# Kernel optimization log

Measured on AMD Instinct MI355X. Metric: run time of the kernel, lower is better.

The kernel has to match this reference:

```python
import jax, jax.numpy as jnp
import numpy as np


def setup_inputs() -> dict:
    key = jax.random.key(0)
    k1, k2, k3 = jax.random.split(key, 3)
    B, C_in, H, W = 32, 128, 56, 56
    C_out, ksz = 256, 3
    x = jax.random.normal(k1, (B, C_in, H, W), dtype=jnp.float32)
    weight = jax.random.normal(k2, (C_out, C_in, ksz, ksz), dtype=jnp.float32) * 0.05
    bias = jax.random.normal(k3, (C_out,), dtype=jnp.float32)
    return {"x": x, "weight": weight, "bias": bias}


PADDING = 1
GROUPS = 1


def reference(x, weight, bias):
    # Same math as the manual pad+unfold+einsum: a standard stride-1 grouped
    # conv2d with symmetric zero padding. Expressed as implicit-GEMM conv.
    out = jax.lax.conv_general_dilated(
        x, weight,
        window_strides=(1, 1),
        padding=[(PADDING, PADDING), (PADDING, PADDING)],
        dimension_numbers=("NCHW", "OIHW", "NCHW"),
        feature_group_count=GROUPS,
    )
    out = out + bias[None, :, None, None]
    return out
```

## Files before the change

kernel.cpp:

```cpp
#include <hip/hip_runtime.h>
#include <stdint.h>

#define BATCH 32
#define CIN   128
#define HH    56
#define WW    56
#define COUT  256
#define HP    58
#define WP    58

typedef __attribute__((ext_vector_type(8))) short short8;
typedef __attribute__((ext_vector_type(4))) float floatx4;

#define GLOAD_LDS16(gptr, lptr)                                          \
  __builtin_amdgcn_global_load_lds(                                      \
      (const __attribute__((address_space(1))) void*)(gptr),             \
      (__attribute__((address_space(3))) void*)(lptr), 16, 0, 0)

__device__ __forceinline__ unsigned short f32_to_bf16(float f) {
  unsigned int u = __float_as_uint(f);
  u = u + 0x7fffu + ((u >> 16) & 1u);
  return (unsigned short)(u >> 16);
}
__device__ __forceinline__ unsigned int pack2(float a, float b) {
  return (unsigned int)f32_to_bf16(a) | ((unsigned int)f32_to_bf16(b) << 16);
}


__global__ void pad_transpose_kernel(const float* __restrict__ x,
                                     unsigned short* __restrict__ xpt) {
  const int blk = blockIdx.x;
  const int b = blk / HP;
  const int i = blk - b * HP;
  const int t = threadIdx.x;
  unsigned short* dst = xpt + (size_t)blk * (WP * CIN);

  if (i == 0 || i == HP - 1) {
    const uint4 z = {0, 0, 0, 0};
    for (int idx = t; idx < 928; idx += 256)
      *(uint4*)(dst + (size_t)idx * 8) = z;
    return;
  }

  __shared__ float tile[CIN * 59];
  tile[(t >> 1) * 59 + (t & 1) * 57] = 0.0f;
  {
    const int ci = t >> 1;
    const int seg = t & 1;
    const float* row =
        x + (((size_t)b * CIN + ci) * HH + (i - 1)) * WW + seg * 28;
    float* trow = tile + ci * 59 + 1 + seg * 28;
#pragma unroll
    for (int q = 0; q < 7; ++q) {
      const float4 v = *(const float4*)(row + q * 4);
      trow[q * 4 + 0] = v.x;
      trow[q * 4 + 1] = v.y;
      trow[q * 4 + 2] = v.z;
      trow[q * 4 + 3] = v.w;
    }
  }
  __syncthreads();
  for (int idx = t; idx < 928; idx += 256) {
    const int j = idx >> 4;
    const int ci0 = (idx & 15) * 8;
    uint4 pk;
    pk.x = pack2(tile[(ci0 + 0) * 59 + j], tile[(ci0 + 1) * 59 + j]);
    pk.y = pack2(tile[(ci0 + 2) * 59 + j], tile[(ci0 + 3) * 59 + j]);
    pk.z = pack2(tile[(ci0 + 4) * 59 + j], tile[(ci0 + 5) * 59 + j]);
    pk.w = pack2(tile[(ci0 + 6) * 59 + j], tile[(ci0 + 7) * 59 + j]);
    *(uint4*)(dst + (size_t)idx * 8) = pk;
  }
}

__global__ void weight_transpose_kernel(const float* __restrict__ wsrc,
                                        unsigned short* __restrict__ wt) {
  const int o8 = blockIdx.x * 256 + threadIdx.x;
  const int r = o8 >> 12;
  const int rem = o8 & 4095;
  const int co = rem >> 4;
  const int ci0 = (rem & 15) * 8;
  const float* s = wsrc + ((size_t)co * CIN + ci0) * 9 + r;
  uint4 pk;
  pk.x = pack2(s[0 * 9], s[1 * 9]);
  pk.y = pack2(s[2 * 9], s[3 * 9]);
  pk.z = pack2(s[4 * 9], s[5 * 9]);
  pk.w = pack2(s[6 * 9], s[7 * 9]);
  *(uint4*)(wt + (size_t)o8 * 8) = pk;
}

__global__ __launch_bounds__(256, 2) void conv_gemm_kernel(
    const unsigned short* __restrict__ xpt,
    const unsigned short* __restrict__ wt,
    const float* __restrict__ bias,
    float* __restrict__ out) {
  __shared__ __align__(16) uint32_t smem[16384];
  short* const S = (short*)smem;
  float* const ep = (float*)smem;

  const int g = blockIdx.x;
  const int xcd = g & 7;
  const int jj = g >> 3;
  const int nt = jj & 1;
  const int mt = (jj >> 1) * 8 + xcd;
  const int b = mt / 28;
  const int h0 = (mt - b * 28) * 2;
  const int co0 = nt * 128;

  const int t = threadIdx.x;
  const int lane = t & 63;
  const int wv = t >> 6;
  const int mw = wv & 1;
  const int nw = wv >> 1;
  const int laneM = lane & 15;
  const int laneKg = lane >> 4;
  const int sw = (laneM & 3) ^ ((laneM >> 2) & 3);
  const int xk = (laneKg ^ sw) * 8;
  const int rowreg = laneKg * 4;

  const unsigned short* ag[2];
  const unsigned short* bg[2];
#pragma unroll
  for (int c = 0; c < 2; ++c) {
    const int u = c * 256 + t;
    const int mm = u >> 2;
    const int smm = (mm & 3) ^ ((mm >> 2) & 3);
    const int j8 = (((u & 3) ^ smm) * 8);
    const int hp0 = h0 + (mm >> 6);
    const int wc0 = mm & 63;
    ag[c] = xpt + ((size_t)((b * HP + hp0) * WP + wc0)) * CIN + j8;
    bg[c] = wt + (size_t)(co0 + mm) * CIN + j8;
  }
  const int dA = wv * 512;

  floatx4 acc[4][4] = {};

  auto stageK = [&](int kk) {
    const int r = kk >> 2;
    const int dh = (r * 11) >> 5;
    const int dw = r - dh * 3;
    const int aoff = (dh * WP + dw) * CIN + (kk & 3) * 32;
    const int boff = r * (COUT * CIN) + (kk & 3) * 32;
    short* const base = S + (kk & 3) * 8192;
    GLOAD_LDS16(ag[0] + aoff, base + dA);
    GLOAD_LDS16(ag[1] + aoff, base + 2048 + dA);
    GLOAD_LDS16(bg[0] + boff, base + 4096 + dA);
    GLOAD_LDS16(bg[1] + boff, base + 4096 + 2048 + dA);
  };

  stageK(0);
  stageK(1);
  asm volatile("s_waitcnt vmcnt(4)" ::: "memory");
  __builtin_amdgcn_s_barrier();
  __builtin_amdgcn_sched_barrier(0);

  for (int kk = 0; kk < 36; ++kk) {
    const short* Ab = S + (kk & 3) * 8192;
    const short* Bb = Ab + 4096;
    short8 af[4], bfr[4];
#pragma unroll
    for (int mi = 0; mi < 4; ++mi)
      af[mi] = *(const short8*)&Ab[(mw * 64 + mi * 16 + laneM) * 32 + xk];
#pragma unroll
    for (int ni = 0; ni < 4; ++ni)
      bfr[ni] = *(const short8*)&Bb[(nw * 64 + ni * 16 + laneM) * 32 + xk];
    if (kk < 34) stageK(kk + 2);
    __builtin_amdgcn_s_setprio(1);
#pragma unroll
    for (int mi = 0; mi < 4; ++mi)
#pragma unroll
      for (int ni = 0; ni < 4; ++ni)
        acc[mi][ni] = __builtin_amdgcn_mfma_f32_16x16x32_bf16(
            af[mi], bfr[ni], acc[mi][ni], 0, 0, 0);
    __builtin_amdgcn_s_setprio(0);
    if (kk < 34)
      asm volatile("s_waitcnt vmcnt(4)" ::: "memory");
    else
      asm volatile("s_waitcnt vmcnt(0)" ::: "memory");
    __builtin_amdgcn_s_barrier();
    __builtin_amdgcn_sched_barrier(0);
  }

  for (int ni = 0; ni < 4; ++ni) {
    __syncthreads();
#pragma unroll
    for (int mi = 0; mi < 4; ++mi)
      *(float4*)&ep[(nw * 16 + laneM) * 132 + mw * 64 + mi * 16 + rowreg] =
          *(float4*)&acc[mi][ni];
    __syncthreads();
#pragma unroll
    for (int rr = 0; rr < 16; ++rr) {
      const int rowid = wv * 16 + rr;
      const int cg = rowid >> 1;
      const int hh = rowid & 1;
      const int co = co0 + (cg >> 4) * 64 + ni * 16 + (cg & 15);
      const float bv = bias[co];
      if (lane < WW) {
        out[(((size_t)b * COUT + co) * HH + h0 + hh) * WW + lane] =
            ep[cg * 132 + hh * 64 + lane] + bv;
      }
    }
  }
}

__global__ void naive_conv_kernel(const float* __restrict__ x,
                                  const float* __restrict__ wgt,
                                  const float* __restrict__ bias,
                                  float* __restrict__ out, long n) {
  long idx = (long)blockIdx.x * 256 + threadIdx.x;
  if (idx >= n) return;
  int w = (int)(idx % WW);
  long q = idx / WW;
  int h = (int)(q % HH);
  q /= HH;
  int co = (int)(q % COUT);
  int b = (int)(q / COUT);
  float s = bias[co];
  for (int ci = 0; ci < CIN; ++ci) {
    const float* xp = x + (((size_t)b * CIN + ci) * HH) * WW;
    const float* wp = wgt + ((size_t)co * CIN + ci) * 9;
    for (int dh = 0; dh < 3; ++dh) {
      int hh = h + dh - 1;
      if (hh < 0 || hh >= HH) continue;
      for (int dw = 0; dw < 3; ++dw) {
        int ww2 = w + dw - 1;
        if (ww2 < 0 || ww2 >= WW) continue;
        s += xp[hh * WW + ww2] * wp[dh * 3 + dw];
      }
    }
  }
  out[idx] = s;
}

extern "C" void kernel_launch(void* const* d_in, const int* in_sizes, int n_in,
                              void* d_out, int out_size, void* d_ws,
                              size_t ws_size, hipStream_t stream) {
  const float* x = (const float*)d_in[0];
  const float* wgt = (const float*)d_in[1];
  const float* bias = (const float*)d_in[2];
  float* out = (float*)d_out;

  const size_t XPT = (size_t)BATCH * HP * WP * CIN;
  const size_t SLACK = 1024;
  const size_t WT = (size_t)9 * COUT * CIN;
  const size_t need = (XPT + SLACK + WT) * sizeof(unsigned short);

  if (ws_size >= need) {
    unsigned short* xpt = (unsigned short*)d_ws;
    unsigned short* wtp = xpt + XPT + SLACK;
    hipLaunchKernelGGL(pad_transpose_kernel, dim3(BATCH * HP), dim3(256), 0,
                       stream, x, xpt);
    hipLaunchKernelGGL(weight_transpose_kernel, dim3(144), dim3(256), 0,
                       stream, wgt, wtp);
    hipLaunchKernelGGL(conv_gemm_kernel, dim3(896 * 2), dim3(256), 0, stream,
                       xpt, wtp, bias, out);
  } else {
    long n = (long)out_size;
    hipLaunchKernelGGL(naive_conv_kernel, dim3((unsigned)((n + 255) / 256)),
                       dim3(256), 0, stream, x, wgt, bias, out, n);
  }
}
```

Measured before the change: 220.6 us.

## Load weight fragments directly into registers and halve LDS for higher occupancy

The weight (B) operand no longer goes through LDS. Each wave loads its B fragments straight from global memory into registers and double-buffers them across two K-steps, while only the activation (A) tiles are staged in LDS. This halves the LDS footprint, so launch bounds move from two to three blocks per CU, and it removes the LDS writes and reads for B. In exchange each wave issues more global/L2 loads for weights, with no sharing across waves in a block. Correct ordering of the A-tile LDS reads now depends on the compiler's implicit vmcnt waits for the register loads.

```diff
diff --git a/kernel.cpp b/kernel.cpp
--- a/kernel.cpp
+++ b/kernel.cpp
@@ -88,12 +88,12 @@
   *(uint4*)(wt + (size_t)o8 * 8) = pk;
 }
 
-__global__ __launch_bounds__(256, 2) void conv_gemm_kernel(
+__global__ __launch_bounds__(256, 3) void conv_gemm_kernel(
     const unsigned short* __restrict__ xpt,
     const unsigned short* __restrict__ wt,
     const float* __restrict__ bias,
     float* __restrict__ out) {
-  __shared__ __align__(16) uint32_t smem[16384];
+  __shared__ __align__(16) uint32_t smem[8192];
   short* const S = (short*)smem;
   float* const ep = (float*)smem;
 
@@ -118,66 +118,89 @@
   const int rowreg = laneKg * 4;
 
   const unsigned short* ag[2];
-  const unsigned short* bg[2];
 #pragma unroll
   for (int c = 0; c < 2; ++c) {
     const int u = c * 256 + t;
     const int mm = u >> 2;
     const int smm = (mm & 3) ^ ((mm >> 2) & 3);
-    const int j8 = (((u & 3) ^ smm) * 8);
-    const int hp0 = h0 + (mm >> 6);
-    const int wc0 = mm & 63;
-    ag[c] = xpt + ((size_t)((b * HP + hp0) * WP + wc0)) * CIN + j8;
-    bg[c] = wt + (size_t)(co0 + mm) * CIN + j8;
+    const int j8 = ((u & 3) ^ smm) * 8;
+    ag[c] =
+        xpt + ((size_t)((b * HP + h0 + (mm >> 6)) * WP + (mm & 63))) * CIN + j8;
   }
   const int dA = wv * 512;
 
+  const unsigned short* wb =
+      wt + (size_t)(co0 + nw * 64 + laneM) * CIN + laneKg * 8;
+
   floatx4 acc[4][4] = {};
-
-  auto stageK = [&](int kk) {
+  short8 af[4], bfA[4], bfB[4];
+
+  auto stageA = [&](int kk) {
     const int r = kk >> 2;
     const int dh = (r * 11) >> 5;
     const int dw = r - dh * 3;
     const int aoff = (dh * WP + dw) * CIN + (kk & 3) * 32;
-    const int boff = r * (COUT * CIN) + (kk & 3) * 32;
-    short* const base = S + (kk & 3) * 8192;
+    short* const base = S + (kk & 3) * 4096;
     GLOAD_LDS16(ag[0] + aoff, base + dA);
     GLOAD_LDS16(ag[1] + aoff, base + 2048 + dA);
-    GLOAD_LDS16(bg[0] + boff, base + 4096 + dA);
-    GLOAD_LDS16(bg[1] + boff, base + 4096 + 2048 + dA);
-  };
-
-  stageK(0);
-  stageK(1);
-  asm volatile("s_waitcnt vmcnt(4)" ::: "memory");
+  };
+  auto loadB = [&](int kk, short8* bf) {
+    const unsigned short* p = wb + (kk >> 2) * (COUT * CIN) + (kk & 3) * 32;
+#pragma unroll
+    for (int ni = 0; ni < 4; ++ni)
+      bf[ni] = *(const short8*)(p + ni * 16 * CIN);
+  };
+  auto frags = [&](int kk) {
+    const short* Ab = S + (kk & 3) * 4096;
+#pragma unroll
+    for (int mi = 0; mi < 4; ++mi)
+      af[mi] = *(const short8*)&Ab[(mw * 64 + mi * 16 + laneM) * 32 + xk];
+  };
+  auto mfma16 = [&](short8* bf) {
+#pragma unroll
+    for (int mi = 0; mi < 4; ++mi)
+#pragma unroll
+      for (int ni = 0; ni < 4; ++ni)
+        acc[mi][ni] = __builtin_amdgcn_mfma_f32_16x16x32_bf16(
+            af[mi], bf[ni], acc[mi][ni], 0, 0, 0);
+  };
+
+  stageA(0);
+  stageA(1);
+  __builtin_amdgcn_sched_barrier(0);
+  loadB(0, bfA);
+  __builtin_amdgcn_sched_barrier(0);
+  asm volatile("s_waitcnt vmcnt(6)" ::: "memory");
   __builtin_amdgcn_s_barrier();
   __builtin_amdgcn_sched_barrier(0);
 
-  for (int kk = 0; kk < 36; ++kk) {
-    const short* Ab = S + (kk & 3) * 8192;
-    const short* Bb = Ab + 4096;
-    short8 af[4], bfr[4];
-#pragma unroll
-    for (int mi = 0; mi < 4; ++mi)
-      af[mi] = *(const short8*)&Ab[(mw * 64 + mi * 16 + laneM) * 32 + xk];
-#pragma unroll
-    for (int ni = 0; ni < 4; ++ni)
-      bfr[ni] = *(const short8*)&Bb[(nw * 64 + ni * 16 + laneM) * 32 + xk];
-    if (kk < 34) stageK(kk + 2);
+  for (int k2 = 0; k2 < 18; ++k2) {
+    const int kk = k2 * 2;
+    const bool more = (k2 < 17);
+    frags(kk);
+    if (more) stageA(kk + 2);
+    __builtin_amdgcn_sched_barrier(0);
+    loadB(kk + 1, bfB);
+    __builtin_amdgcn_sched_barrier(0);
     __builtin_amdgcn_s_setprio(1);
-#pragma unroll
-    for (int mi = 0; mi < 4; ++mi)
-#pragma unroll
-      for (int ni = 0; ni < 4; ++ni)
-        acc[mi][ni] = __builtin_amdgcn_mfma_f32_16x16x32_bf16(
-            af[mi], bfr[ni], acc[mi][ni], 0, 0, 0);
+    mfma16(bfA);
     __builtin_amdgcn_s_setprio(0);
-    if (kk < 34)
-      asm volatile("s_waitcnt vmcnt(4)" ::: "memory");
-    else
-      asm volatile("s_waitcnt vmcnt(0)" ::: "memory");
+    asm volatile("s_waitcnt vmcnt(6)" ::: "memory");
     __builtin_amdgcn_s_barrier();
     __builtin_amdgcn_sched_barrier(0);
+    frags(kk + 1);
+    if (more) stageA(kk + 3);
+    __builtin_amdgcn_sched_barrier(0);
+    if (more) loadB(kk + 2, bfA);
+    __builtin_amdgcn_sched_barrier(0);
+    __builtin_amdgcn_s_setprio(1);
+    mfma16(bfB);
+    __builtin_amdgcn_s_setprio(0);
+    if (more) {
+      asm volatile("s_waitcnt vmcnt(6)" ::: "memory");
+      __builtin_amdgcn_s_barrier();
+      __builtin_amdgcn_sched_barrier(0);
+    }
   }
 
   for (int ni = 0; ni < 4; ++ni) {
```

Result: slower. 277.1 us (+25.6%).

## Enlarge conv GEMM tile to 256x256 with 512 threads and 3-deep prefetch

Applied to the files above, without the earlier changes.

Each block now covers 4 output rows by all 256 output channels (256x256 tile) using 8 waves, each computing 128x64. This replaces the earlier 128x128 tile with 4 waves. The goal is to halve global and LDS traffic per FLOP and remove the duplicate activation loads across the two channel halves. The pipeline prefetches 3 K-slices ahead instead of 2 and drops the final barrier. It also removes the XOR LDS swizzle, which risks bank conflicts on fragment reads, and it doubles LDS (128KB) and accumulator register use, which may limit occupancy. The grid falls to 448 blocks, which could cause wave-quantization imbalance.

```diff
diff --git a/kernel.cpp b/kernel.cpp
--- a/kernel.cpp
+++ b/kernel.cpp
@@ -88,51 +88,44 @@
   *(uint4*)(wt + (size_t)o8 * 8) = pk;
 }
 
-__global__ __launch_bounds__(256, 2) void conv_gemm_kernel(
+__global__ __launch_bounds__(512, 2) void conv_gemm_kernel(
     const unsigned short* __restrict__ xpt,
     const unsigned short* __restrict__ wt,
     const float* __restrict__ bias,
     float* __restrict__ out) {
-  __shared__ __align__(16) uint32_t smem[16384];
+  __shared__ __align__(16) uint32_t smem[32768];
   short* const S = (short*)smem;
   float* const ep = (float*)smem;
 
   const int g = blockIdx.x;
-  const int xcd = g & 7;
-  const int jj = g >> 3;
-  const int nt = jj & 1;
-  const int mt = (jj >> 1) * 8 + xcd;
-  const int b = mt / 28;
-  const int h0 = (mt - b * 28) * 2;
-  const int co0 = nt * 128;
+  const int mt = (g & 7) * 56 + (g >> 3);
+  const int b = mt / 14;
+  const int h0 = (mt - b * 14) * 4;
 
   const int t = threadIdx.x;
   const int lane = t & 63;
   const int wv = t >> 6;
-  const int mw = wv & 1;
-  const int nw = wv >> 1;
+  const int mw = wv >> 2;
+  const int nw = wv & 3;
   const int laneM = lane & 15;
   const int laneKg = lane >> 4;
-  const int sw = (laneM & 3) ^ ((laneM >> 2) & 3);
-  const int xk = (laneKg ^ sw) * 8;
   const int rowreg = laneKg * 4;
 
   const unsigned short* ag[2];
   const unsigned short* bg[2];
 #pragma unroll
   for (int c = 0; c < 2; ++c) {
-    const int u = c * 256 + t;
+    const int u = c * 512 + t;
     const int mm = u >> 2;
-    const int smm = (mm & 3) ^ ((mm >> 2) & 3);
-    const int j8 = (((u & 3) ^ smm) * 8);
-    const int hp0 = h0 + (mm >> 6);
-    const int wc0 = mm & 63;
-    ag[c] = xpt + ((size_t)((b * HP + hp0) * WP + wc0)) * CIN + j8;
-    bg[c] = wt + (size_t)(co0 + mm) * CIN + j8;
-  }
-  const int dA = wv * 512;
-
-  floatx4 acc[4][4] = {};
+    const int p = u & 3;
+    ag[c] = xpt +
+            ((size_t)((b * HP + h0 + (mm >> 6)) * WP + (mm & 63))) * CIN +
+            p * 8;
+    bg[c] = wt + (size_t)mm * CIN + p * 8;
+  }
+  const int dW = wv * 512;
+
+  floatx4 acc[8][4] = {};
 
   auto stageK = [&](int kk) {
     const int r = kk >> 2;
@@ -140,63 +133,72 @@
     const int dw = r - dh * 3;
     const int aoff = (dh * WP + dw) * CIN + (kk & 3) * 32;
     const int boff = r * (COUT * CIN) + (kk & 3) * 32;
-    short* const base = S + (kk & 3) * 8192;
-    GLOAD_LDS16(ag[0] + aoff, base + dA);
-    GLOAD_LDS16(ag[1] + aoff, base + 2048 + dA);
-    GLOAD_LDS16(bg[0] + boff, base + 4096 + dA);
-    GLOAD_LDS16(bg[1] + boff, base + 4096 + 2048 + dA);
+    short* const slot = S + (kk & 3) * 16384;
+    GLOAD_LDS16(ag[0] + aoff, slot + dW);
+    GLOAD_LDS16(ag[1] + aoff, slot + 4096 + dW);
+    GLOAD_LDS16(bg[0] + boff, slot + 8192 + dW);
+    GLOAD_LDS16(bg[1] + boff, slot + 12288 + dW);
   };
 
   stageK(0);
   stageK(1);
-  asm volatile("s_waitcnt vmcnt(4)" ::: "memory");
+  stageK(2);
+  __builtin_amdgcn_sched_barrier(0);
+  asm volatile("s_waitcnt vmcnt(8)" ::: "memory");
   __builtin_amdgcn_s_barrier();
   __builtin_amdgcn_sched_barrier(0);
 
   for (int kk = 0; kk < 36; ++kk) {
-    const short* Ab = S + (kk & 3) * 8192;
-    const short* Bb = Ab + 4096;
-    short8 af[4], bfr[4];
-#pragma unroll
-    for (int mi = 0; mi < 4; ++mi)
-      af[mi] = *(const short8*)&Ab[(mw * 64 + mi * 16 + laneM) * 32 + xk];
+    const short* slot = S + (kk & 3) * 16384;
+    short8 af[8], bf[4];
+#pragma unroll
+    for (int mi = 0; mi < 8; ++mi)
+      af[mi] =
+          *(const short8*)&slot[(mw * 128 + mi * 16 + laneM) * 32 + laneKg * 8];
 #pragma unroll
     for (int ni = 0; ni < 4; ++ni)
-      bfr[ni] = *(const short8*)&Bb[(nw * 64 + ni * 16 + laneM) * 32 + xk];
-    if (kk < 34) stageK(kk + 2);
+      bf[ni] = *(const short8*)&slot[8192 +
+                                     (nw * 64 + ni * 16 + laneM) * 32 +
+                                     laneKg * 8];
+    if (kk <= 32) stageK(kk + 3);
+    __builtin_amdgcn_sched_barrier(0);
     __builtin_amdgcn_s_setprio(1);
 #pragma unroll
-    for (int mi = 0; mi < 4; ++mi)
+    for (int mi = 0; mi < 8; ++mi)
 #pragma unroll
       for (int ni = 0; ni < 4; ++ni)
         acc[mi][ni] = __builtin_amdgcn_mfma_f32_16x16x32_bf16(
-            af[mi], bfr[ni], acc[mi][ni], 0, 0, 0);
+            af[mi], bf[ni], acc[mi][ni], 0, 0, 0);
     __builtin_amdgcn_s_setprio(0);
-    if (kk < 34)
+    if (kk <= 32)
+      asm volatile("s_waitcnt vmcnt(8)" ::: "memory");
+    else if (kk == 33)
       asm volatile("s_waitcnt vmcnt(4)" ::: "memory");
-    else
+    else if (kk == 34)
       asm volatile("s_waitcnt vmcnt(0)" ::: "memory");
-    __builtin_amdgcn_s_barrier();
-    __builtin_amdgcn_sched_barrier(0);
+    if (kk < 35) {
+      __builtin_amdgcn_s_barrier();
+      __builtin_amdgcn_sched_barrier(0);
+    }
   }
 
   for (int ni = 0; ni < 4; ++ni) {
     __syncthreads();
 #pragma unroll
-    for (int mi = 0; mi < 4; ++mi)
-      *(float4*)&ep[(nw * 16 + laneM) * 132 + mw * 64 + mi * 16 + rowreg] =
+    for (int mi = 0; mi < 8; ++mi)
+      *(float4*)&ep[(nw * 16 + laneM) * 260 + mw * 128 + mi * 16 + rowreg] =
           *(float4*)&acc[mi][ni];
     __syncthreads();
 #pragma unroll
-    for (int rr = 0; rr < 16; ++rr) {
-      const int rowid = wv * 16 + rr;
-      const int cg = rowid >> 1;
-      const int hh = rowid & 1;
-      const int co = co0 + (cg >> 4) * 64 + ni * 16 + (cg & 15);
+    for (int rr = 0; rr < 32; ++rr) {
+      const int rid = wv * 32 + rr;
+      const int cp = rid >> 2;
+      const int hq2 = rid & 3;
+      const int co = (cp >> 4) * 64 + ni * 16 + (cp & 15);
       const float bv = bias[co];
       if (lane < WW) {
-        out[(((size_t)b * COUT + co) * HH + h0 + hh) * WW + lane] =
-            ep[cg * 132 + hh * 64 + lane] + bv;
+        out[(((size_t)b * COUT + co) * HH + h0 + hq2) * WW + lane] =
+            ep[cp * 260 + hq2 * 64 + lane] + bv;
       }
     }
   }
@@ -251,7 +253,7 @@
                        stream, x, xpt);
     hipLaunchKernelGGL(weight_transpose_kernel, dim3(144), dim3(256), 0,
                        stream, wgt, wtp);
-    hipLaunchKernelGGL(conv_gemm_kernel, dim3(896 * 2), dim3(256), 0, stream,
+    hipLaunchKernelGGL(conv_gemm_kernel, dim3(448), dim3(512), 0, stream,
                        xpt, wtp, bias, out);
   } else {
     long n = (long)out_size;
```

Result: slower. 274.3 us (+24.3%).
